# Kernel optimization log

Hardware: AMD Instinct MI355X
Metric: run time of the kernel (lower is better)

## Reference

```python
import jax, jax.numpy as jnp
import numpy as np

NEG_SLOPE = 0.2    # DenseGATConv attention leaky_relu slope (PyG default)
ACT_SLOPE = 0.01   # block activation LeakyReLU slope
HEADS = 3


def setup_inputs() -> dict:
    key = jax.random.key(0)
    B, N, D0, D1, D2, H = 512, 128, 128, 64, 64, HEADS
    ks = jax.random.split(key, 7)
    x = jax.random.normal(ks[0], (B * N, D0), jnp.float32)
    # equal-sized graphs: sorted graph ids, N atoms per graph
    batch_mask = jnp.repeat(jnp.arange(B, dtype=jnp.int32), N)
    s0 = 1.0 / np.sqrt(D0)
    s1 = 1.0 / np.sqrt(D1)
    s2 = 1.0 / np.sqrt(D2)
    W1 = jax.random.normal(ks[1], (D0, H * D1), jnp.float32) * s0
    att_src1 = jax.random.normal(ks[2], (H, D1), jnp.float32) * s1
    att_dst1 = jax.random.normal(ks[3], (H, D1), jnp.float32) * s1
    b1 = jnp.zeros((D1,), jnp.float32)
    W2 = jax.random.normal(ks[4], (D1, H * D2), jnp.float32) * s1
    att_src2 = jax.random.normal(ks[5], (H, D2), jnp.float32) * s2
    att_dst2 = jax.random.normal(ks[6], (H, D2), jnp.float32) * s2
    b2 = jnp.zeros((D2,), jnp.float32)
    return dict(x=x, batch_mask=batch_mask, W1=W1, att_src1=att_src1,
                att_dst1=att_dst1, b1=b1, W2=W2, att_src2=att_src2,
                att_dst2=att_dst2, b2=b2, batch_size=B, n_max=N)


def _dense_gat(x, adj, W, a_src, a_dst, b):
    # x: [B, N, Din], adj: [B, N, N] (self-loops already set). concat=False.
    B, N, _ = x.shape
    H, C = a_src.shape
    h = (x @ W).reshape(B, N, H, C)                       # lin (no bias)
    a_s = jnp.einsum('bnhc,hc->bnh', h, a_src)            # per-node src score
    a_d = jnp.einsum('bnhc,hc->bnh', h, a_dst)            # per-node dst score
    alpha = a_s[:, None, :, :] + a_d[:, :, None, :]       # [B, i, j, H]
    alpha = jax.nn.leaky_relu(alpha, NEG_SLOPE)
    alpha = jnp.where(adj[..., None] == 0, -jnp.inf, alpha)
    alpha = jax.nn.softmax(alpha, axis=2)                 # over source j
    out = jnp.einsum('bijh,bjhc->bihc', alpha, h)         # [B, N, H, C]
    return out.mean(axis=2) + b                           # concat=False -> head mean


def reference(x, batch_mask, W1, att_src1, att_dst1, b1,
              W2, att_src2, att_dst2, b2, batch_size, n_max):
    total, D0 = x.shape
    counts = jnp.bincount(batch_mask, length=batch_size)          # atoms per graph
    starts = jnp.cumsum(counts) - counts
    pos = jnp.arange(total) - starts[batch_mask]                  # slot within graph
    # to_dense_batch
    xd = jnp.zeros((batch_size, n_max, D0), x.dtype).at[batch_mask, pos].set(x)
    node_in = jnp.arange(n_max)[None, :] < counts[:, None]        # [B, N] valid mask
    # block adjacency: fully connected within each graph, diag zeroed...
    adj = (node_in[:, :, None] & node_in[:, None, :]).astype(x.dtype)
    # ...then DenseGATConv add_loop=True re-sets the full diagonal to 1
    adj = jnp.where(jnp.eye(n_max, dtype=bool), jnp.asarray(1.0, x.dtype), adj)
    h = _dense_gat(xd, adj, W1, att_src1, att_dst1, b1)
    h = jax.nn.leaky_relu(h, ACT_SLOPE)
    h = _dense_gat(h, adj, W2, att_src2, att_dst2, b2)
    h = jax.nn.leaky_relu(h, ACT_SLOPE)
    return jnp.sum(h, axis=1)                                     # sum pooling -> [B, D2]
```

## Files before the change

kernel.cpp:

```cpp
#include <hip/hip_runtime.h>
#include <stdint.h>

#define NROW 128

typedef __attribute__((ext_vector_type(8))) __bf16 bf16x8;
typedef __attribute__((ext_vector_type(4))) float  f32x4;

static __device__ __forceinline__ uint16_t f2bf(float f) {
    union { float f; uint32_t i; } v; v.f = f;
    uint32_t x = v.i;
    return (uint16_t)((x + 0x7FFFu + ((x >> 16) & 1u)) >> 16);
}
static __device__ __forceinline__ uint16_t bfbits(float f) {
    __bf16 h = (__bf16)f;
    union { __bf16 h; uint16_t u; } c; c.h = h; return c.u;
}
static __device__ __forceinline__ float fexp2(float x) {
#if __has_builtin(__builtin_amdgcn_exp2f)
    return __builtin_amdgcn_exp2f(x);
#else
    return exp2f(x);
#endif
}
static __device__ __forceinline__ float frcp(float x) {
#if __has_builtin(__builtin_amdgcn_rcpf)
    return __builtin_amdgcn_rcpf(x);
#else
    return 1.0f / x;
#endif
}

__global__ __launch_bounds__(256)
void prep_kernel(const float* __restrict__ W1, const float* __restrict__ as1,
                 const float* __restrict__ ad1,
                 const float* __restrict__ W2, const float* __restrict__ as2,
                 const float* __restrict__ ad2,
                 uint16_t* __restrict__ wT1x, uint16_t* __restrict__ wT2x)
{
    constexpr float LOG2E = 1.4426950408889634f;
    int bid = blockIdx.x, t = threadIdx.x;
    if (bid < 96) {
        int idx = bid * 256 + t;
        int c = idx >> 7, k = idx & 127;
        wT1x[c * 128 + k] = f2bf(W1[k * 192 + c]);
    } else if (bid < 144) {
        int idx = (bid - 96) * 256 + t;
        int c = idx >> 6, k = idx & 63;
        wT2x[c * 64 + k] = f2bf(W2[k * 192 + c]);
    } else if (bid == 144) {
#pragma unroll
        for (int e = 0; e < 3; ++e) {
            int idx = t + e * 256;
            if (idx < 768) {
                int j = idx >> 7, k = idx & 127, hd = j >> 1;
                const float* av = (j & 1) ? ad1 : as1;
                float s = 0.f;
                for (int c = 0; c < 64; ++c)
                    s += W1[k * 192 + hd * 64 + c] * av[hd * 64 + c];
                wT1x[(192 + j) * 128 + k] = f2bf(s * LOG2E);
            }
        }
#pragma unroll
        for (int e = 0; e < 5; ++e) {
            int idx = t + e * 256;
            if (idx < 1280) wT1x[198 * 128 + idx] = 0;
        }
    } else {
#pragma unroll
        for (int e = 0; e < 2; ++e) {
            int idx = t + e * 256;
            if (idx < 384) {
                int j = idx >> 6, k = idx & 63, hd = j >> 1;
                const float* av = (j & 1) ? ad2 : as2;
                float s = 0.f;
                for (int c = 0; c < 64; ++c)
                    s += W2[k * 192 + hd * 64 + c] * av[hd * 64 + c];
                wT2x[(192 + j) * 64 + k] = f2bf(s * LOG2E);
            }
        }
#pragma unroll
        for (int e = 0; e < 3; ++e) {
            int idx = t + e * 256;
            if (idx < 640) wT2x[198 * 64 + idx] = 0;
        }
    }
}

#define HS 136
#define S2 72

static __device__ __forceinline__
void scores_and_hT(const f32x4* hacc, uint16_t* hT, float* as_s, float* ad_s,
                   int i0, int lr, int lg)
{
    if (lr < 6) {
        float* dst = (lr & 1) ? ad_s : as_s;
        int hd = lr >> 1;
#pragma unroll
        for (int r = 0; r < 4; ++r)
            dst[hd * 128 + i0 + lg * 4 + r] = hacc[12][r];
    }
#pragma unroll
    for (int f = 0; f < 12; ++f) {
        uint32_t p0 = (uint32_t)bfbits(hacc[f][0]) | ((uint32_t)bfbits(hacc[f][1]) << 16);
        uint32_t p1 = (uint32_t)bfbits(hacc[f][2]) | ((uint32_t)bfbits(hacc[f][3]) << 16);
        *(uint2*)&hT[(f * 16 + lr) * HS + i0 + lg * 4] = make_uint2(p0, p1);
    }
}

static __device__ __forceinline__
void softmax_pv(const uint16_t* hT, const float* as_s, const float* ad_s,
                f32x4* oacc, int i0, int l, int lr, int lg)
{
#pragma unroll
    for (int f = 0; f < 4; ++f) oacc[f] = (f32x4){0.f, 0.f, 0.f, 0.f};

    float mxh[3];
#pragma unroll
    for (int hd = 0; hd < 3; ++hd)
        mxh[hd] = fmaxf(as_s[hd * 128 + l], as_s[hd * 128 + l + 64]);
#pragma unroll
    for (int off = 1; off < 64; off <<= 1)
#pragma unroll
        for (int hd = 0; hd < 3; ++hd) mxh[hd] = fmaxf(mxh[hd], __shfl_xor(mxh[hd], off));

    for (int hd = 0; hd < 3; ++hd) {
        float ad = ad_s[hd * 128 + i0 + lr];
        float m0 = mxh[hd] + ad;
        float mi = fmaxf(m0, 0.2f * m0);
        bf16x8 ap[4];
        float zp = 0.f;
#pragma unroll
        for (int q = 0; q < 4; ++q) {
            float4 s0 = *(const float4*)&as_s[hd * 128 + q * 32 + lg * 8];
            float4 s1 = *(const float4*)&as_s[hd * 128 + q * 32 + lg * 8 + 4];
            float sv[8] = {s0.x, s0.y, s0.z, s0.w, s1.x, s1.y, s1.z, s1.w};
#pragma unroll
            for (int m = 0; m < 8; ++m) {
                float tt = sv[m] + ad;
                tt = fmaxf(tt, 0.2f * tt);
                float ev = fexp2(tt - mi);
                zp += ev;
                ap[q][m] = (__bf16)ev;
            }
        }
        zp += __shfl_xor(zp, 16);
        zp += __shfl_xor(zp, 32);
        float inv = frcp(3.0f * zp);

        f32x4 tacc[4];
#pragma unroll
        for (int f = 0; f < 4; ++f) tacc[f] = (f32x4){0.f, 0.f, 0.f, 0.f};
#pragma unroll
        for (int q = 0; q < 4; ++q)
#pragma unroll
            for (int f = 0; f < 4; ++f) {
                bf16x8 bfv = *(const bf16x8*)&hT[(hd * 64 + f * 16 + lr) * HS + q * 32 + lg * 8];
                tacc[f] = __builtin_amdgcn_mfma_f32_16x16x32_bf16(ap[q], bfv, tacc[f], 0, 0, 0);
            }
        float invr[4];
#pragma unroll
        for (int r = 0; r < 4; ++r) invr[r] = __shfl(inv, lg * 4 + r);
#pragma unroll
        for (int f = 0; f < 4; ++f)
#pragma unroll
            for (int r = 0; r < 4; ++r) oacc[f][r] += tacc[f][r] * invr[r];
    }
}

__global__ __launch_bounds__(512, 4)
void fused_kernel(const float* __restrict__ x,
                  const uint16_t* __restrict__ wT1g, const uint16_t* __restrict__ wT2g,
                  const float* __restrict__ b1g, const float* __restrict__ b2g,
                  float* __restrict__ outp)
{
    __shared__ __align__(16) uint16_t buf[208 * HS];
    __shared__ __align__(16) float as_s[3 * 128];
    __shared__ __align__(16) float ad_s[3 * 128];
    __shared__ float bia[2][64];
    __shared__ float pool_s[8 * 64];

    uint16_t* wT1l = buf;
    uint16_t* hT   = buf;
    uint16_t* x2T  = buf;
    uint16_t* wT2l = buf + 128 * S2;

    const int b = blockIdx.x, t = threadIdx.x;
    const int w = t >> 6, l = t & 63, lr = l & 15, lg = l >> 4;
    const int i0 = w * 16;

    bf16x8 afr[4];
    {
        const float* xg = x + ((long)b * NROW + i0 + lr) * 128;
        float4 r0[4], r1[4];
#pragma unroll
        for (int q = 0; q < 4; ++q) {
            r0[q] = *(const float4*)(xg + q * 32 + lg * 8);
            r1[q] = *(const float4*)(xg + q * 32 + lg * 8 + 4);
        }
#pragma unroll
        for (int q = 0; q < 4; ++q) {
            bf16x8 a;
            a[0] = (__bf16)r0[q].x; a[1] = (__bf16)r0[q].y;
            a[2] = (__bf16)r0[q].z; a[3] = (__bf16)r0[q].w;
            a[4] = (__bf16)r1[q].x; a[5] = (__bf16)r1[q].y;
            a[6] = (__bf16)r1[q].z; a[7] = (__bf16)r1[q].w;
            afr[q] = a;
        }
    }
#pragma unroll
    for (int p = 0; p < 7; ++p) {
        int idx = t + p * 512;
        if (idx < 3328) {
            int row = idx >> 4, c8 = (idx & 15) * 8;
            *(uint4*)&wT1l[row * HS + c8] = *(const uint4*)(wT1g + row * 128 + c8);
        }
    }
    if (t < 64) bia[0][t] = b1g[t];
    else if (t < 128) bia[1][t - 64] = b2g[t - 64];
    __syncthreads();

    f32x4 hacc[13];
#pragma unroll
    for (int f = 0; f < 13; ++f) hacc[f] = (f32x4){0.f, 0.f, 0.f, 0.f};
#pragma unroll
    for (int q = 0; q < 4; ++q) {
#pragma unroll
        for (int f = 0; f < 13; ++f) {
            bf16x8 bfv = *(const bf16x8*)&wT1l[(f * 16 + lr) * HS + q * 32 + lg * 8];
            hacc[f] = __builtin_amdgcn_mfma_f32_16x16x32_bf16(afr[q], bfv, hacc[f], 0, 0, 0);
        }
    }
    __syncthreads();

    scores_and_hT(hacc, hT, as_s, ad_s, i0, lr, lg);
    __syncthreads();

    uint4 wpre[4];
#pragma unroll
    for (int p = 0; p < 3; ++p) {
        int idx = t + p * 512; int row = idx >> 3; int c8 = (idx & 7) * 8;
        wpre[p] = *(const uint4*)(wT2g + row * 64 + c8);
    }
    if (t < 128) {
        int idx = t + 1536; int row = idx >> 3; int c8 = (idx & 7) * 8;
        wpre[3] = *(const uint4*)(wT2g + row * 64 + c8);
    }

    f32x4 oacc[4];
    softmax_pv(hT, as_s, ad_s, oacc, i0, l, lr, lg);
    __syncthreads();

    {
#pragma unroll
        for (int f = 0; f < 4; ++f) {
            int c = f * 16 + lr;
            float bv = bia[0][c];
#pragma unroll
            for (int r = 0; r < 4; ++r) {
                float v = oacc[f][r] + bv;
                v = fmaxf(v, 0.01f * v);
                x2T[(i0 + lg * 4 + r) * S2 + c] = bfbits(v);
            }
        }
#pragma unroll
        for (int p = 0; p < 3; ++p) {
            int idx = t + p * 512; int row = idx >> 3; int c8 = (idx & 7) * 8;
            *(uint4*)&wT2l[row * S2 + c8] = wpre[p];
        }
        if (t < 128) {
            int idx = t + 1536; int row = idx >> 3; int c8 = (idx & 7) * 8;
            *(uint4*)&wT2l[row * S2 + c8] = wpre[3];
        }
    }
    __syncthreads();

#pragma unroll
    for (int f = 0; f < 13; ++f) hacc[f] = (f32x4){0.f, 0.f, 0.f, 0.f};
#pragma unroll
    for (int q = 0; q < 2; ++q) {
        bf16x8 af = *(const bf16x8*)&x2T[(i0 + lr) * S2 + q * 32 + lg * 8];
#pragma unroll
        for (int f = 0; f < 13; ++f) {
            bf16x8 bfv = *(const bf16x8*)&wT2l[(f * 16 + lr) * S2 + q * 32 + lg * 8];
            hacc[f] = __builtin_amdgcn_mfma_f32_16x16x32_bf16(af, bfv, hacc[f], 0, 0, 0);
        }
    }
    __syncthreads();

    scores_and_hT(hacc, hT, as_s, ad_s, i0, lr, lg);
    __syncthreads();

    softmax_pv(hT, as_s, ad_s, oacc, i0, l, lr, lg);

#pragma unroll
    for (int f = 0; f < 4; ++f) {
        int c = f * 16 + lr;
        float bv = bia[1][c];
        float s = 0.f;
#pragma unroll
        for (int r = 0; r < 4; ++r) {
            float v = oacc[f][r] + bv;
            v = fmaxf(v, 0.01f * v);
            s += v;
        }
        s += __shfl_xor(s, 16);
        s += __shfl_xor(s, 32);
        if (lg == 0) pool_s[w * 64 + c] = s;
    }
    __syncthreads();
    if (t < 64) {
        float s = 0.f;
#pragma unroll
        for (int q = 0; q < 8; ++q) s += pool_s[q * 64 + t];
        outp[(long)b * 64 + t] = s;
    }
}

extern "C" void kernel_launch(void* const* d_in, const int* in_sizes, int n_in,
                              void* d_out, int out_size, void* d_ws, size_t ws_size,
                              hipStream_t stream)
{
    const float* x   = (const float*)d_in[0];
    const float* W1  = (const float*)d_in[2];
    const float* as1 = (const float*)d_in[3];
    const float* ad1 = (const float*)d_in[4];
    const float* b1  = (const float*)d_in[5];
    const float* W2  = (const float*)d_in[6];
    const float* as2 = (const float*)d_in[7];
    const float* ad2 = (const float*)d_in[8];
    const float* b2  = (const float*)d_in[9];

    uint16_t* wT1x = (uint16_t*)d_ws;
    uint16_t* wT2x = wT1x + 208 * 128;

    prep_kernel<<<146, 256, 0, stream>>>(W1, as1, ad1, W2, as2, ad2, wT1x, wT2x);
    fused_kernel<<<512, 512, 0, stream>>>(x, wT1x, wT2x, b1, b2, (float*)d_out);
}
```

Baseline: 127.7 us.

## Read GEMM weights from global, swizzle hT LDS layout, drop softmax max reduction

The weight matrices for both projection GEMMs are now read straight from global memory (L2-cached) as MFMA B fragments instead of being staged into LDS, which removes the weight staging copies and several block-wide barriers. The hT buffer switches from padded rows to an XOR-swizzled 256-byte row layout to avoid bank conflicts while using less LDS. The per-row softmax max reduction over shuffles is replaced with a fixed offset of 16 in the exponent, and the leaky-relu is folded into a single fmax of two affine forms. The fixed offset assumes scores stay within fp32 exp2 range, so it risks overflow or underflow for inputs with larger score magnitudes. The reduced LDS footprint may also allow more resident blocks.

```diff
diff --git a/kernel.cpp b/kernel.cpp
--- a/kernel.cpp
+++ b/kernel.cpp
@@ -86,7 +86,10 @@
     }
 }
 
-#define HS 136
+static __device__ __forceinline__ uint32_t hT_off(int row, int colbytes) {
+    uint32_t bo = (uint32_t)(row * 256 + colbytes);
+    return bo ^ (uint32_t)((row & 7) << 4);
+}
 #define S2 72
 
 static __device__ __forceinline__
@@ -104,30 +107,22 @@
     for (int f = 0; f < 12; ++f) {
         uint32_t p0 = (uint32_t)bfbits(hacc[f][0]) | ((uint32_t)bfbits(hacc[f][1]) << 16);
         uint32_t p1 = (uint32_t)bfbits(hacc[f][2]) | ((uint32_t)bfbits(hacc[f][3]) << 16);
-        *(uint2*)&hT[(f * 16 + lr) * HS + i0 + lg * 4] = make_uint2(p0, p1);
+        *(uint2*)((char*)hT + hT_off(f * 16 + lr, (i0 + lg * 4) * 2)) = make_uint2(p0, p1);
     }
 }
 
 static __device__ __forceinline__
 void softmax_pv(const uint16_t* hT, const float* as_s, const float* ad_s,
-                f32x4* oacc, int i0, int l, int lr, int lg)
+                f32x4* oacc, int i0, int lr, int lg)
 {
 #pragma unroll
     for (int f = 0; f < 4; ++f) oacc[f] = (f32x4){0.f, 0.f, 0.f, 0.f};
 
-    float mxh[3];
-#pragma unroll
-    for (int hd = 0; hd < 3; ++hd)
-        mxh[hd] = fmaxf(as_s[hd * 128 + l], as_s[hd * 128 + l + 64]);
-#pragma unroll
-    for (int off = 1; off < 64; off <<= 1)
-#pragma unroll
-        for (int hd = 0; hd < 3; ++hd) mxh[hd] = fmaxf(mxh[hd], __shfl_xor(mxh[hd], off));
-
+#pragma unroll
     for (int hd = 0; hd < 3; ++hd) {
-        float ad = ad_s[hd * 128 + i0 + lr];
-        float m0 = mxh[hd] + ad;
-        float mi = fmaxf(m0, 0.2f * m0);
+        float ad  = ad_s[hd * 128 + i0 + lr];
+        float adm = ad - 16.0f;
+        float adn = 0.2f * ad - 16.0f;
         bf16x8 ap[4];
         float zp = 0.f;
 #pragma unroll
@@ -137,9 +132,7 @@
             float sv[8] = {s0.x, s0.y, s0.z, s0.w, s1.x, s1.y, s1.z, s1.w};
 #pragma unroll
             for (int m = 0; m < 8; ++m) {
-                float tt = sv[m] + ad;
-                tt = fmaxf(tt, 0.2f * tt);
-                float ev = fexp2(tt - mi);
+                float ev = fexp2(fmaxf(sv[m] + adm, __builtin_fmaf(sv[m], 0.2f, adn)));
                 zp += ev;
                 ap[q][m] = (__bf16)ev;
             }
@@ -155,7 +148,8 @@
         for (int q = 0; q < 4; ++q)
 #pragma unroll
             for (int f = 0; f < 4; ++f) {
-                bf16x8 bfv = *(const bf16x8*)&hT[(hd * 64 + f * 16 + lr) * HS + q * 32 + lg * 8];
+                bf16x8 bfv = *(const bf16x8*)((const char*)hT +
+                                 hT_off(hd * 64 + f * 16 + lr, q * 64 + lg * 16));
                 tacc[f] = __builtin_amdgcn_mfma_f32_16x16x32_bf16(ap[q], bfv, tacc[f], 0, 0, 0);
             }
         float invr[4];
@@ -174,19 +168,17 @@
                   const float* __restrict__ b1g, const float* __restrict__ b2g,
                   float* __restrict__ outp)
 {
-    __shared__ __align__(16) uint16_t buf[208 * HS];
+    __shared__ __align__(16) char smem[49152];
     __shared__ __align__(16) float as_s[3 * 128];
     __shared__ __align__(16) float ad_s[3 * 128];
-    __shared__ float bia[2][64];
+    __shared__ float bia[128];
     __shared__ float pool_s[8 * 64];
 
-    uint16_t* wT1l = buf;
-    uint16_t* hT   = buf;
-    uint16_t* x2T  = buf;
-    uint16_t* wT2l = buf + 128 * S2;
+    uint16_t* hT  = (uint16_t*)smem;
+    uint16_t* x2T = (uint16_t*)smem;
 
     const int b = blockIdx.x, t = threadIdx.x;
-    const int w = t >> 6, l = t & 63, lr = l & 15, lg = l >> 4;
+    const int w = t >> 6, lr = t & 15, lg = (t >> 4) & 3;
     const int i0 = w * 16;
 
     bf16x8 afr[4];
@@ -208,95 +200,72 @@
             afr[q] = a;
         }
     }
-#pragma unroll
-    for (int p = 0; p < 7; ++p) {
-        int idx = t + p * 512;
-        if (idx < 3328) {
-            int row = idx >> 4, c8 = (idx & 15) * 8;
-            *(uint4*)&wT1l[row * HS + c8] = *(const uint4*)(wT1g + row * 128 + c8);
-        }
-    }
-    if (t < 64) bia[0][t] = b1g[t];
-    else if (t < 128) bia[1][t - 64] = b2g[t - 64];
-    __syncthreads();
+    if (t < 64) bia[t] = b1g[t];
+    else if (t < 128) bia[t] = b2g[t - 64];
 
     f32x4 hacc[13];
 #pragma unroll
     for (int f = 0; f < 13; ++f) hacc[f] = (f32x4){0.f, 0.f, 0.f, 0.f};
-#pragma unroll
-    for (int q = 0; q < 4; ++q) {
-#pragma unroll
-        for (int f = 0; f < 13; ++f) {
-            bf16x8 bfv = *(const bf16x8*)&wT1l[(f * 16 + lr) * HS + q * 32 + lg * 8];
-            hacc[f] = __builtin_amdgcn_mfma_f32_16x16x32_bf16(afr[q], bfv, hacc[f], 0, 0, 0);
-        }
-    }
-    __syncthreads();
+    {
+        const uint16_t* wb = wT1g + lr * 128 + lg * 8;
+#pragma unroll
+        for (int q = 0; q < 4; ++q)
+#pragma unroll
+            for (int f = 0; f < 13; ++f) {
+                bf16x8 bfv = *(const bf16x8*)(wb + f * 2048 + q * 32);
+                hacc[f] = __builtin_amdgcn_mfma_f32_16x16x32_bf16(afr[q], bfv, hacc[f], 0, 0, 0);
+            }
+    }
 
     scores_and_hT(hacc, hT, as_s, ad_s, i0, lr, lg);
     __syncthreads();
 
-    uint4 wpre[4];
-#pragma unroll
-    for (int p = 0; p < 3; ++p) {
-        int idx = t + p * 512; int row = idx >> 3; int c8 = (idx & 7) * 8;
-        wpre[p] = *(const uint4*)(wT2g + row * 64 + c8);
-    }
-    if (t < 128) {
-        int idx = t + 1536; int row = idx >> 3; int c8 = (idx & 7) * 8;
-        wpre[3] = *(const uint4*)(wT2g + row * 64 + c8);
-    }
-
     f32x4 oacc[4];
-    softmax_pv(hT, as_s, ad_s, oacc, i0, l, lr, lg);
-    __syncthreads();
-
-    {
-#pragma unroll
-        for (int f = 0; f < 4; ++f) {
-            int c = f * 16 + lr;
-            float bv = bia[0][c];
-#pragma unroll
-            for (int r = 0; r < 4; ++r) {
-                float v = oacc[f][r] + bv;
-                v = fmaxf(v, 0.01f * v);
-                x2T[(i0 + lg * 4 + r) * S2 + c] = bfbits(v);
-            }
-        }
-#pragma unroll
-        for (int p = 0; p < 3; ++p) {
-            int idx = t + p * 512; int row = idx >> 3; int c8 = (idx & 7) * 8;
-            *(uint4*)&wT2l[row * S2 + c8] = wpre[p];
-        }
-        if (t < 128) {
-            int idx = t + 1536; int row = idx >> 3; int c8 = (idx & 7) * 8;
-            *(uint4*)&wT2l[row * S2 + c8] = wpre[3];
-        }
-    }
-    __syncthreads();
-
-#pragma unroll
-    for (int f = 0; f < 13; ++f) hacc[f] = (f32x4){0.f, 0.f, 0.f, 0.f};
-#pragma unroll
-    for (int q = 0; q < 2; ++q) {
-        bf16x8 af = *(const bf16x8*)&x2T[(i0 + lr) * S2 + q * 32 + lg * 8];
-#pragma unroll
-        for (int f = 0; f < 13; ++f) {
-            bf16x8 bfv = *(const bf16x8*)&wT2l[(f * 16 + lr) * S2 + q * 32 + lg * 8];
-            hacc[f] = __builtin_amdgcn_mfma_f32_16x16x32_bf16(af, bfv, hacc[f], 0, 0, 0);
-        }
-    }
-    __syncthreads();
-
-    scores_and_hT(hacc, hT, as_s, ad_s, i0, lr, lg);
-    __syncthreads();
-
-    softmax_pv(hT, as_s, ad_s, oacc, i0, l, lr, lg);
+    softmax_pv(hT, as_s, ad_s, oacc, i0, lr, lg);
+    __syncthreads();
 
 #pragma unroll
     for (int f = 0; f < 4; ++f) {
         int c = f * 16 + lr;
-        float bv = bia[1][c];
+        float bv = bia[c];
+#pragma unroll
+        for (int r = 0; r < 4; ++r) {
+            float v = oacc[f][r] + bv;
+            v = fmaxf(v, 0.01f * v);
+            x2T[(i0 + lg * 4 + r) * S2 + c] = bfbits(v);
+        }
+    }
+    asm volatile("s_waitcnt lgkmcnt(0)" ::: "memory");
+    __builtin_amdgcn_sched_barrier(0);
+
+    bf16x8 af2[2];
+#pragma unroll
+    for (int q = 0; q < 2; ++q)
+        af2[q] = *(const bf16x8*)&x2T[(i0 + lr) * S2 + q * 32 + lg * 8];
+    __syncthreads();
+
+#pragma unroll
+    for (int f = 0; f < 13; ++f) hacc[f] = (f32x4){0.f, 0.f, 0.f, 0.f};
+    {
+        const uint16_t* wb = wT2g + lr * 64 + lg * 8;
+#pragma unroll
+        for (int q = 0; q < 2; ++q)
+#pragma unroll
+            for (int f = 0; f < 13; ++f) {
+                bf16x8 bfv = *(const bf16x8*)(wb + f * 1024 + q * 32);
+                hacc[f] = __builtin_amdgcn_mfma_f32_16x16x32_bf16(af2[q], bfv, hacc[f], 0, 0, 0);
+            }
+    }
+
+    scores_and_hT(hacc, hT, as_s, ad_s, i0, lr, lg);
+    __syncthreads();
+
+    softmax_pv(hT, as_s, ad_s, oacc, i0, lr, lg);
+
+#pragma unroll
+    for (int f = 0; f < 4; ++f) {
+        int c = f * 16 + lr;
+        float bv = bia[64 + c];
         float s = 0.f;
 #pragma unroll
         for (int r = 0; r < 4; ++r) {
```

After: 155.0 us. 21.4% more time.
